# Kernel optimization log

Measured on AMD Instinct MI355X. Metric: run time of the kernel, lower is better.

Reference implementation:

```python
import jax, jax.numpy as jnp
import numpy as np
from jax import lax

# Paraformer-large streaming decoder dims
L, H, DFF, NH, DK, K, V, T, S, CKV, LB = 16, 512, 2048, 4, 128, 11, 8404, 64, 2048, 256, 256


def _ln(x, g, b, eps=1e-5):
    m = jnp.mean(x, axis=-1, keepdims=True)
    var = jnp.mean((x - m) ** 2, axis=-1, keepdims=True)
    return (x - m) * lax.rsqrt(var + eps) * g + b


def setup_inputs() -> dict:
    key = jax.random.key(0)
    ks = jax.random.split(key, 20)
    w = lambda k, shp: jax.random.normal(k, shp, jnp.float32) * 0.02
    return {
        "encoder_out": jax.random.normal(ks[0], (1, S, H), jnp.float32),
        "list_frame": jax.random.normal(ks[1], (1, T, H), jnp.float32),
        "fsmn_cache": jax.random.normal(ks[2], (L, 1, H, K - 1), jnp.float32),
        "key_cache": jax.random.normal(ks[3], (L, NH, DK, CKV), jnp.float32),
        "value_cache": jax.random.normal(ks[4], (L, NH, CKV, DK), jnp.float32),
        "norm1_g": jnp.ones((L, H)), "norm1_b": jnp.zeros((L, H)),
        "norm2_g": jnp.ones((L, H)), "norm2_b": jnp.zeros((L, H)),
        "norm3_g": jnp.ones((L, H)), "norm3_b": jnp.zeros((L, H)),
        "ffn_norm_g": jnp.ones((L, DFF)), "ffn_norm_b": jnp.zeros((L, DFF)),
        "w1": w(ks[5], (L, H, DFF)), "b1": jnp.zeros((L, DFF)),
        "w2": w(ks[6], (L, DFF, H)),  # bias-free in FunASR DecoderSANM
        "fsmn_w": w(ks[7], (L, H, K)),  # depthwise conv, groups=H, no bias
        "qw": w(ks[8], (L, H, H)), "qb": jnp.zeros((L, H)),
        "kvw": w(ks[9], (L, H, 2 * H)), "kvb": jnp.zeros((L, 2 * H)),
        "ow": w(ks[10], (L, H, H)), "ob": jnp.zeros((L, H)),
        "d3_norm1_g": jnp.ones((H,)), "d3_norm1_b": jnp.zeros((H,)),
        "d3_w1": w(ks[11], (H, DFF)), "d3_b1": jnp.zeros((DFF,)),
        "d3_ffn_norm_g": jnp.ones((DFF,)), "d3_ffn_norm_b": jnp.zeros((DFF,)),
        "d3_w2": w(ks[12], (DFF, H)),
        "after_norm_g": jnp.ones((H,)), "after_norm_b": jnp.zeros((H,)),
        "out_w": w(ks[13], (H, V)), "out_b": jnp.zeros((V,)),
        "list_frame_len": T,
    }


def reference(encoder_out, list_frame, fsmn_cache, key_cache, value_cache,
              norm1_g, norm1_b, norm2_g, norm2_b, norm3_g, norm3_b,
              ffn_norm_g, ffn_norm_b, w1, b1, w2, fsmn_w, qw, qb, kvw, kvb, ow, ob,
              d3_norm1_g, d3_norm1_b, d3_w1, d3_b1, d3_ffn_norm_g, d3_ffn_norm_b, d3_w2,
              after_norm_g, after_norm_b, out_w, out_b, list_frame_len):
    enc = encoder_out[0]  # [S, H]
    scale = DK ** -0.5

    def layer_fn(lf, p):
        (fc, kc, vc, n1g, n1b, n2g, n2b, n3g, n3b, fng, fnb,
         W1, B1, W2, FW, QW, QB, KVW, KVB, OW, OB) = p
        residual = lf
        y = _ln(lf, n1g, n1b)
        y = _ln(jax.nn.relu(y @ W1 + B1), fng, fnb) @ W2
        y = _ln(y, n2g, n2b)
        # cache concat; slice [look_back:] with look_back = -(K-1)-T keeps all K-1+T cols
        x_cat = jnp.concatenate([fc, jnp.swapaxes(y, 1, 2)], axis=-1)  # [1, H, K-1+T]
        conv = lax.conv_general_dilated(
            x_cat, FW[:, None, :], (1,), 'VALID',
            dimension_numbers=('NCH', 'OIH', 'NCH'), feature_group_count=H)  # [1, H, T]
        x = jnp.swapaxes(conv, 1, 2) + y + residual
        residual = x
        q = (_ln(x, n3g, n3b)[0] @ QW + QB).reshape(-1, NH, DK).transpose(1, 0, 2) * scale  # [h, T, dk]
        kv = enc @ KVW + KVB  # [S, 2H]
        k = kv[:, :H].reshape(-1, NH, DK).transpose(1, 2, 0)  # [h, dk, S]
        v = kv[:, H:].reshape(-1, NH, DK).transpose(1, 0, 2)  # [h, S, dk]
        k = jnp.concatenate([kc, k], axis=2)  # [h, dk, CKV+S]
        v = jnp.concatenate([vc, v], axis=1)  # [h, CKV+S, dk]
        attn = jax.nn.softmax(jnp.einsum('htd,hds->hts', q, k), axis=-1)
        ctx = jnp.einsum('hts,hsd->htd', attn, v).transpose(1, 0, 2).reshape(1, -1, H)
        lf = residual + ctx @ OW + OB
        return lf, (x_cat, k[:, :, -LB:], v[:, -LB:, :])

    layer_params = (fsmn_cache, key_cache, value_cache, norm1_g, norm1_b, norm2_g, norm2_b,
                    norm3_g, norm3_b, ffn_norm_g, ffn_norm_b, w1, b1, w2, fsmn_w,
                    qw, qb, kvw, kvb, ow, ob)
    lf, (save_fsmn, save_keys, save_values) = lax.scan(layer_fn, list_frame, layer_params)
    x = _ln(lf, d3_norm1_g, d3_norm1_b)
    x = _ln(jax.nn.relu(x @ d3_w1 + d3_b1), d3_ffn_norm_g, d3_ffn_norm_b) @ d3_w2
    logits = _ln(x, after_norm_g, after_norm_b) @ out_w + out_b
    max_logit_ids = jnp.argmax(logits, axis=-1).astype(jnp.int32)
    return save_fsmn, save_keys, save_values, max_logit_ids
```

## Files before the change

### kernel.cpp

```cpp
#include <hip/hip_runtime.h>

constexpr int LAY = 16, HID = 512, FF = 2048, NHD = 4, DKH = 128, KW = 11,
              VOC = 8404, TT = 64, SEQ = 2048, LBN = 256;

#define SWZ(row, e) ((e) ^ ((((row) >> 2) & 7) << 2))

__global__ void diag_k(float* __restrict__ p, float v) { p[threadIdx.x] = v; }

__global__ __launch_bounds__(256) void redln_k(
    const float* __restrict__ P, int N, int nch,
    const float* __restrict__ bias, const float* __restrict__ res, int relu,
    const float* __restrict__ g, const float* __restrict__ b,
    float* __restrict__ out1, float* __restrict__ out2) {
  __shared__ float buf[2048];
  __shared__ float red[256];
  const int m = blockIdx.x, tid = threadIdx.x;
  float s = 0.f;
  for (int n = tid; n < N; n += 256) {
    const float* p = P + (size_t)m * N + n;
    float v = 0.f;
    for (int c = 0; c < nch; ++c) v += p[(size_t)c * 64 * N];
    if (bias) v += bias[n];
    if (res) v += res[(size_t)m * N + n];
    if (relu) v = fmaxf(v, 0.f);
    if (out1) out1[(size_t)m * N + n] = v;
    buf[n] = v; s += v;
  }
  red[tid] = s; __syncthreads();
  for (int st = 128; st > 0; st >>= 1) { if (tid < st) red[tid] += red[tid + st]; __syncthreads(); }
  const float mean = red[0] / N;
  __syncthreads();
  float vs = 0.f;
  for (int n = tid; n < N; n += 256) { float d = buf[n] - mean; vs += d * d; }
  red[tid] = vs; __syncthreads();
  for (int st = 128; st > 0; st >>= 1) { if (tid < st) red[tid] += red[tid + st]; __syncthreads(); }
  const float inv = rsqrtf(red[0] / N + 1e-5f);
  for (int n = tid; n < N; n += 256)
    out2[(size_t)m * N + n] = (buf[n] - mean) * inv * g[n] + b[n];
}

__global__ __launch_bounds__(256) void gemm32_nn(
    const float* __restrict__ A, int lda, long sA,
    const float* __restrict__ B, int ldb, long sB,
    int N, int Kd, int nch,
    float* __restrict__ part, long pzs, int coff,
    int aCh, long aChS,
    const float* __restrict__ rsA, const float* __restrict__ bvA, long pzA) {
  __shared__ float As[64][64];
  __shared__ float Bs[64][40];
  const int tid = threadIdx.x;
  const int l16r = tid >> 4, l16c = tid & 15;
  const int lr = tid >> 3, lc = tid & 7;
  const int bn = blockIdx.x * 32;
  const int chunk = blockIdx.y;
  const int z = blockIdx.z;
  A += (long)z * sA; B += (long)z * sB;
  float acc[2][4] = {};
  const int ktiles = Kd >> 6;
  const int fa = (l16c & 7) << 2;
  for (int kt = chunk; kt < ktiles; kt += nch) {
    const int k0 = kt << 6;
    __syncthreads();
#pragma unroll
    for (int i = 0; i < 4; ++i) {
      const int r = l16r + 16 * i;
      float4 av;
      if (rsA) {
        const int kcol = k0 + l16c * 4;
        const int zz = kcol >> 7, d = kcol & 127;
        const float* ap = A + (size_t)zz * pzA + (size_t)r * 128 + d;
        av = *(const float4*)ap;
        for (int c = 1; c < aCh; ++c) {
          const float4 t2 = *(const float4*)(ap + (size_t)c * aChS);
          av.x += t2.x; av.y += t2.y; av.z += t2.z; av.w += t2.w;
        }
        const float4 bb = *(const float4*)(bvA + kcol);
        const float rv = rsA[zz * 64 + r];
        av.x += rv * bb.x; av.y += rv * bb.y; av.z += rv * bb.z; av.w += rv * bb.w;
      } else {
        const float* ap = A + (size_t)r * lda + k0 + l16c * 4;
        av = *(const float4*)ap;
        for (int c = 1; c < aCh; ++c) {
          const float4 t2 = *(const float4*)(ap + (size_t)c * aChS);
          av.x += t2.x; av.y += t2.y; av.z += t2.z; av.w += t2.w;
        }
      }
      As[l16c * 4 + 0][r ^ fa] = av.x; As[l16c * 4 + 1][r ^ fa] = av.y;
      As[l16c * 4 + 2][r ^ fa] = av.z; As[l16c * 4 + 3][r ^ fa] = av.w;
    }
#pragma unroll
    for (int i = 0; i < 2; ++i) {
      const int rb = lr + 32 * i;
      const float4 bv = *(const float4*)(B + (size_t)(k0 + rb) * ldb + bn + lc * 4);
      *(float4*)(&Bs[rb][lc * 4]) = bv;
    }
    __syncthreads();
#pragma unroll 8
    for (int kk = 0; kk < 64; ++kk) {
      const int fk = ((kk >> 2) & 7) << 2;
      const float2 a = *(const float2*)(&As[kk][(lr * 2) ^ fk]);
      const float4 b = *(const float4*)(&Bs[kk][lc * 4]);
      acc[0][0] += a.x * b.x; acc[0][1] += a.x * b.y; acc[0][2] += a.x * b.z; acc[0][3] += a.x * b.w;
      acc[1][0] += a.y * b.x; acc[1][1] += a.y * b.y; acc[1][2] += a.y * b.z; acc[1][3] += a.y * b.w;
    }
  }
  float* P = part + (size_t)z * pzs + (size_t)(coff + chunk) * 64 * N;
#pragma unroll
  for (int i = 0; i < 2; ++i) {
    const int m = lr * 2 + i;
#pragma unroll
    for (int j = 0; j < 4; ++j) P[(size_t)m * N + bn + lc * 4 + j] = acc[i][j];
  }
}

__global__ __launch_bounds__(256) void gemm_nn(
    const float* __restrict__ A, int lda, long sA,
    const float* __restrict__ B, int ldb, long sB,
    float* __restrict__ C, int ldc, long sC,
    const float* __restrict__ bias,
    const float* __restrict__ res, int ldres,
    int N, int Kd, int flags, int nch,
    float* __restrict__ part, long pzs, int coff,
    int aCh, long aChS) {
  __shared__ float As[64][64];
  __shared__ float Bs[64][64];
  const int tid = threadIdx.x;
  const int lr = tid >> 4, lc = tid & 15;
  const int bn = blockIdx.x * 64;
  const int chunk = blockIdx.y;
  const int z = blockIdx.z;
  A += (long)z * sA; B += (long)z * sB; C += (long)z * sC;
  float acc[4][4] = {};
  const int ktiles = Kd >> 6;
  const int fa = (lc & 7) << 2;
  for (int kt = chunk; kt < ktiles; kt += nch) {
    const int k0 = kt << 6;
    __syncthreads();
#pragma unroll
    for (int i = 0; i < 4; ++i) {
      const int r = lr + 16 * i;
      const float* ap = A + (size_t)r * lda + k0 + lc * 4;
      float4 av = *(const float4*)ap;
      for (int c = 1; c < aCh; ++c) {
        const float4 t2 = *(const float4*)(ap + (size_t)c * aChS);
        av.x += t2.x; av.y += t2.y; av.z += t2.z; av.w += t2.w;
      }
      As[lc * 4 + 0][r ^ fa] = av.x; As[lc * 4 + 1][r ^ fa] = av.y;
      As[lc * 4 + 2][r ^ fa] = av.z; As[lc * 4 + 3][r ^ fa] = av.w;
      const int n = bn + lc * 4;
      const float* bp = B + (size_t)(k0 + r) * ldb + n;
      float4 bv;
      if (n + 3 < N) bv = *(const float4*)bp;
      else {
        bv.x = (n + 0 < N) ? bp[0] : 0.f;
        bv.y = (n + 1 < N) ? bp[1] : 0.f;
        bv.z = (n + 2 < N) ? bp[2] : 0.f;
        bv.w = (n + 3 < N) ? bp[3] : 0.f;
      }
      *(float4*)(&Bs[r][SWZ(r, lc * 4)]) = bv;
    }
    __syncthreads();
#pragma unroll 8
    for (int kk = 0; kk < 64; ++kk) {
      const int fk = ((kk >> 2) & 7) << 2;
      const float4 a = *(const float4*)(&As[kk][(lr * 4) ^ fk]);
      const float4 b = *(const float4*)(&Bs[kk][(lc * 4) ^ fk]);
      acc[0][0] += a.x * b.x; acc[0][1] += a.x * b.y; acc[0][2] += a.x * b.z; acc[0][3] += a.x * b.w;
      acc[1][0] += a.y * b.x; acc[1][1] += a.y * b.y; acc[1][2] += a.y * b.z; acc[1][3] += a.y * b.w;
      acc[2][0] += a.z * b.x; acc[2][1] += a.z * b.y; acc[2][2] += a.z * b.z; acc[2][3] += a.z * b.w;
      acc[3][0] += a.w * b.x; acc[3][1] += a.w * b.y; acc[3][2] += a.w * b.z; acc[3][3] += a.w * b.w;
    }
  }
  if (part) {
    float* P = part + (size_t)z * pzs + (size_t)(coff + chunk) * 64 * N;
#pragma unroll
    for (int i = 0; i < 4; ++i) {
      const int m = lr * 4 + i;
#pragma unroll
      for (int j = 0; j < 4; ++j) P[(size_t)m * N + bn + lc * 4 + j] = acc[i][j];
    }
    return;
  }
#pragma unroll
  for (int i = 0; i < 4; ++i) {
    const int m = lr * 4 + i;
#pragma unroll
    for (int j = 0; j < 4; ++j) {
      const int n = bn + lc * 4 + j;
      if (n < N) {
        float v = acc[i][j];
        if (bias) v += bias[n];
        if (res) v += res[(size_t)m * ldres + n];
        if (flags & 2) v += C[(size_t)m * ldc + n];
        if (flags & 1) v = fmaxf(v, 0.f);
        C[(size_t)m * ldc + n] = v;
      }
    }
  }
}

__global__ __launch_bounds__(256) void gemm_nt(
    const float* __restrict__ A, int lda, long sA,
    const float* __restrict__ B, int ldb, long sB,
    float* __restrict__ C, int ldc, long sC,
    int N, int Kd, int nch, float* __restrict__ part) {
  __shared__ float As[64][64];
  __shared__ float Bs[64][64];
  const int tid = threadIdx.x;
  const int lr = tid >> 4, lc = tid & 15;
  const int bn = blockIdx.x * 64;
  const int chunk = blockIdx.y;
  const int z = blockIdx.z;
  A += (long)z * sA; B += (long)z * sB; C += (long)z * sC;
  float acc[4][4] = {};
  const int ktiles = Kd >> 6;
  const int fa = (lc & 7) << 2;
  for (int kt = chunk; kt < ktiles; kt += nch) {
    const int k0 = kt << 6;
    __syncthreads();
#pragma unroll
    for (int i = 0; i < 4; ++i) {
      const int r = lr + 16 * i;
      const float4 av = *(const float4*)(A + (size_t)r * lda + k0 + lc * 4);
      As[lc * 4 + 0][r ^ fa] = av.x; As[lc * 4 + 1][r ^ fa] = av.y;
      As[lc * 4 + 2][r ^ fa] = av.z; As[lc * 4 + 3][r ^ fa] = av.w;
      const float4 bv = *(const float4*)(B + (size_t)(bn + r) * ldb + k0 + lc * 4);
      Bs[lc * 4 + 0][r ^ fa] = bv.x; Bs[lc * 4 + 1][r ^ fa] = bv.y;
      Bs[lc * 4 + 2][r ^ fa] = bv.z; Bs[lc * 4 + 3][r ^ fa] = bv.w;
    }
    __syncthreads();
#pragma unroll 8
    for (int kk = 0; kk < 64; ++kk) {
      const int fk = ((kk >> 2) & 7) << 2;
      const float4 a = *(const float4*)(&As[kk][(lr * 4) ^ fk]);
      const float4 b = *(const float4*)(&Bs[kk][(lc * 4) ^ fk]);
      acc[0][0] += a.x * b.x; acc[0][1] += a.x * b.y; acc[0][2] += a.x * b.z; acc[0][3] += a.x * b.w;
      acc[1][0] += a.y * b.x; acc[1][1] += a.y * b.y; acc[1][2] += a.y * b.z; acc[1][3] += a.y * b.w;
      acc[2][0] += a.z * b.x; acc[2][1] += a.z * b.y; acc[2][2] += a.z * b.z; acc[2][3] += a.z * b.w;
      acc[3][0] += a.w * b.x; acc[3][1] += a.w * b.y; acc[3][2] += a.w * b.z; acc[3][3] += a.w * b.w;
    }
  }
  if (chunk == 0) {
#pragma unroll
    for (int i = 0; i < 4; ++i)
#pragma unroll
      for (int j = 0; j < 4; ++j)
        C[(size_t)(lr * 4 + i) * ldc + bn + lc * 4 + j] = acc[i][j];
  } else {
    float* P = part + (size_t)z * (64L * SEQ) + (size_t)(chunk - 1) * 64 * SEQ * NHD;
#pragma unroll
    for (int i = 0; i < 4; ++i)
#pragma unroll
      for (int j = 0; j < 4; ++j)
        P[(size_t)(lr * 4 + i) * SEQ + bn + lc * 4 + j] = acc[i][j];
  }
}

__global__ __launch_bounds__(256) void attn1_k(
    const float* __restrict__ qpart, const float* __restrict__ qbi_l,
    const float* __restrict__ Wkv, const float* __restrict__ kcl,
    float* __restrict__ qp, float* __restrict__ sc,
    int ckv, int sct) {
  __shared__ float As[64][64];
  __shared__ float Bs[64][64];
  const int tid = threadIdx.x;
  const int lr = tid >> 4, lc = tid & 15;
  const int h = blockIdx.z;
  const bool isQp = blockIdx.x < 8;
  const int bn = (isQp ? blockIdx.x : blockIdx.x - 8) * 64;
  const int fa = (lc & 7) << 2;
  float acc[4][4] = {};
  for (int k0 = 0; k0 < DKH; k0 += 64) {
    __syncthreads();
#pragma unroll
    for (int i = 0; i < 4; ++i) {
      const int r = lr + 16 * i;
      const float* ap = qpart + (size_t)r * HID + h * DKH + k0 + lc * 4;
      float4 av = *(const float4*)ap;
      for (int c = 1; c < 8; ++c) {
        const float4 t2 = *(const float4*)(ap + (size_t)c * 64 * HID);
        av.x += t2.x; av.y += t2.y; av.z += t2.z; av.w += t2.w;
      }
      const float4 bb = *(const float4*)(qbi_l + h * DKH + k0 + lc * 4);
      av.x += bb.x; av.y += bb.y; av.z += bb.z; av.w += bb.w;
      As[lc * 4 + 0][r ^ fa] = av.x; As[lc * 4 + 1][r ^ fa] = av.y;
      As[lc * 4 + 2][r ^ fa] = av.z; As[lc * 4 + 3][r ^ fa] = av.w;
      if (isQp) {
        const float4 bv = *(const float4*)(Wkv + (size_t)(bn + r) * (2 * HID) + h * DKH + k0 + lc * 4);
        Bs[lc * 4 + 0][r ^ fa] = bv.x; Bs[lc * 4 + 1][r ^ fa] = bv.y;
        Bs[lc * 4 + 2][r ^ fa] = bv.z; Bs[lc * 4 + 3][r ^ fa] = bv.w;
      } else {
        const float4 bv = *(const float4*)(kcl + ((size_t)h * DKH + k0 + r) * ckv + bn + lc * 4);
        *(float4*)(&Bs[r][SWZ(r, lc * 4)]) = bv;
      }
    }
    __syncthreads();
#pragma unroll 8
    for (int kk = 0; kk < 64; ++kk) {
      const int fk = ((kk >> 2) & 7) << 2;
      const float4 a = *(const float4*)(&As[kk][(lr * 4) ^ fk]);
      const float4 b = *(const float4*)(&Bs[kk][(lc * 4) ^ fk]);
      acc[0][0] += a.x * b.x; acc[0][1] += a.x * b.y; acc[0][2] += a.x * b.z; acc[0][3] += a.x * b.w;
      acc[1][0] += a.y * b.x; acc[1][1] += a.y * b.y; acc[1][2] += a.y * b.z; acc[1][3] += a.y * b.w;
      acc[2][0] += a.z * b.x; acc[2][1] += a.z * b.y; acc[2][2] += a.z * b.z; acc[2][3] += a.z * b.w;
      acc[3][0] += a.w * b.x; acc[3][1] += a.w * b.y; acc[3][2] += a.w * b.z; acc[3][3] += a.w * b.w;
    }
  }
  if (isQp) {
    float* C = qp + (size_t)h * TT * HID;
#pragma unroll
    for (int i = 0; i < 4; ++i)
#pragma unroll
      for (int j = 0; j < 4; ++j)
        C[(size_t)(lr * 4 + i) * HID + bn + lc * 4 + j] = acc[i][j];
  } else {
    float* C = sc + (size_t)h * TT * sct;
#pragma unroll
    for (int i = 0; i < 4; ++i)
#pragma unroll
      for (int j = 0; j < 4; ++j)
        C[(size_t)(lr * 4 + i) * sct + bn + lc * 4 + j] = acc[i][j];
  }
}

__global__ __launch_bounds__(256) void attn2_k(
    const float* __restrict__ sc, const float* __restrict__ vcl,
    const float* __restrict__ enc,
    float* __restrict__ part, float* __restrict__ partE,
    int ckv, int sct, int ncho, long pzc) {
  __shared__ float As[64][64];
  __shared__ float Bs[64][64];
  const int tid = threadIdx.x;
  const int lr = tid >> 4, lc = tid & 15;
  const int h = blockIdx.z;
  const int by = blockIdx.y;
  const bool isOld = blockIdx.x < 2;
  if (isOld && by >= ncho) return;
  if (!isOld && by >= 8) return;
  const float* A;
  const float* Bb;
  int lda, ldb, N, ktiles, nch, bn;
  float* P;
  if (isOld) {
    A = sc + (size_t)h * TT * sct;  lda = sct;
    Bb = vcl + (size_t)h * ckv * DKH; ldb = DKH;
    N = DKH; ktiles = ckv >> 6; nch = ncho; bn = blockIdx.x * 64;
    P = part + (size_t)h * pzc + (size_t)by * 64 * DKH;
  } else {
    A = sc + ckv + (size_t)h * TT * sct; lda = sct;
    Bb = enc; ldb = HID;
    N = HID; ktiles = SEQ >> 6; nch = 8; bn = (blockIdx.x - 2) * 64;
    P = partE + (size_t)h * (8L * 64 * HID) + (size_t)by * 64 * HID;
  }
  const int fa = (lc & 7) << 2;
  float acc[4][4] = {};
  for (int kt = by; kt < ktiles; kt += nch) {
    const int k0 = kt << 6;
    __syncthreads();
#pragma unroll
    for (int i = 0; i < 4; ++i) {
      const int r = lr + 16 * i;
      const float4 av = *(const float4*)(A + (size_t)r * lda + k0 + lc * 4);
      As[lc * 4 + 0][r ^ fa] = av.x; As[lc * 4 + 1][r ^ fa] = av.y;
      As[lc * 4 + 2][r ^ fa] = av.z; As[lc * 4 + 3][r ^ fa] = av.w;
      const float4 bv = *(const float4*)(Bb + (size_t)(k0 + r) * ldb + bn + lc * 4);
      *(float4*)(&Bs[r][SWZ(r, lc * 4)]) = bv;
    }
    __syncthreads();
#pragma unroll 8
    for (int kk = 0; kk < 64; ++kk) {
      const int fk = ((kk >> 2) & 7) << 2;
      const float4 a = *(const float4*)(&As[kk][(lr * 4) ^ fk]);
      const float4 b = *(const float4*)(&Bs[kk][(lc * 4) ^ fk]);
      acc[0][0] += a.x * b.x; acc[0][1] += a.x * b.y; acc[0][2] += a.x * b.z; acc[0][3] += a.x * b.w;
      acc[1][0] += a.y * b.x; acc[1][1] += a.y * b.y; acc[1][2] += a.y * b.z; acc[1][3] += a.y * b.w;
      acc[2][0] += a.z * b.x; acc[2][1] += a.z * b.y; acc[2][2] += a.z * b.z; acc[2][3] += a.z * b.w;
      acc[3][0] += a.w * b.x; acc[3][1] += a.w * b.y; acc[3][2] += a.w * b.z; acc[3][3] += a.w * b.w;
    }
  }
#pragma unroll
  for (int i = 0; i < 4; ++i)
#pragma unroll
    for (int j = 0; j < 4; ++j)
      P[(size_t)(lr * 4 + i) * N + bn + lc * 4 + j] = acc[i][j];
}

__global__ __launch_bounds__(256) void fsmnln_k(
    const float* __restrict__ y4, const float* __restrict__ lfin,
    const float* __restrict__ cache, const float* __restrict__ fw,
    const float* __restrict__ g, const float* __restrict__ b,
    float* __restrict__ xb, float* __restrict__ xcat,
    float* __restrict__ y1out) {
  __shared__ float buf[HID];
  __shared__ float red[256];
  const int t = blockIdx.x, tid = threadIdx.x;
  float s = 0.f;
  for (int h = tid; h < HID; h += 256) {
    float conv = 0.f;
#pragma unroll
    for (int k = 0; k < KW; ++k) {
      const int j = t + k;
      const float xcv = (j < KW - 1) ? cache[h * (KW - 1) + j]
                                     : y4[(size_t)(j - (KW - 1)) * HID + h];
      conv += xcv * fw[h * KW + k];
    }
    const float yv = y4[(size_t)t * HID + h];
    const float x = conv + yv + lfin[(size_t)t * HID + h];
    xb[(size_t)t * HID + h] = x;
    buf[h] = x; s += x;
    xcat[h * (KW - 1 + TT) + (KW - 1) + t] = yv;
    if (t == 0) {
      for (int j2 = 0; j2 < KW - 1; ++j2)
        xcat[h * (KW - 1 + TT) + j2] = cache[h * (KW - 1) + j2];
    }
  }
  red[tid] = s; __syncthreads();
  for (int st = 128; st > 0; st >>= 1) { if (tid < st) red[tid] += red[tid + st]; __syncthreads(); }
  const float mean = red[0] / HID;
  __syncthreads();
  float vs = 0.f;
  for (int h = tid; h < HID; h += 256) { float d = buf[h] - mean; vs += d * d; }
  red[tid] = vs; __syncthreads();
  for (int st = 128; st > 0; st >>= 1) { if (tid < st) red[tid] += red[tid + st]; __syncthreads(); }
  const float inv = rsqrtf(red[0] / HID + 1e-5f);
  for (int h = tid; h < HID; h += 256)
    y1out[(size_t)t * HID + h] = (buf[h] - mean) * inv * g[h] + b[h];
}

__global__ __launch_bounds__(256) void softmax_k(
    float* __restrict__ sc, float* __restrict__ rs,
    const float* __restrict__ qpart, const float* __restrict__ qbi_l,
    const float* __restrict__ kb, const float* __restrict__ partN,
    int cols, int newStart, float alpha) {
  __shared__ float srow[8192];
  __shared__ float red[256];
  const int tid = threadIdx.x;
  const int row = blockIdx.x;
  const int h = row >> 6, t = row & 63;
  sc += (size_t)row * cols;
  const float* pn = partN + (size_t)h * 64 * SEQ + (size_t)t * SEQ;
  float qv = 0.f;
  if (tid < DKH) {
    const float* qp0 = qpart + (size_t)t * HID + h * DKH + tid;
    float q = qp0[0];
    for (int c = 1; c < 8; ++c) q += qp0[(size_t)c * 64 * HID];
    q += qbi_l[h * DKH + tid];
    qv = q * kb[h * DKH + tid];
  }
  red[tid] = qv; __syncthreads();
  for (int st = 64; st > 0; st >>= 1) { if (tid < st) red[tid] += red[tid + st]; __syncthreads(); }
  const float qcv = red[0];
  __syncthreads();
  float m = -3.4e38f;
  for (int c = tid; c < cols; c += 256) {
    float v = sc[c];
    if (c >= newStart) v += pn[c - newStart] + qcv;
    v *= alpha;
    srow[c] = v; m = fmaxf(m, v);
  }
  red[tid] = m; __syncthreads();
  for (int st = 128; st > 0; st >>= 1) { if (tid < st) red[tid] = fmaxf(red[tid], red[tid + st]); __syncthreads(); }
  m = red[0]; __syncthreads();
  float s = 0.f;
  for (int c = tid; c < cols; c += 256) {
    const float e = __expf(srow[c] - m);
    srow[c] = e; s += e;
  }
  red[tid] = s; __syncthreads();
  for (int st = 128; st > 0; st >>= 1) { if (tid < st) red[tid] += red[tid + st]; __syncthreads(); }
  const float inv = 1.f / red[0];
  float ns = 0.f;
  for (int c = tid; c < cols; c += 256) {
    const float p = srow[c] * inv; sc[c] = p;
    if (c >= newStart) ns += p;
  }
  __syncthreads();
  red[tid] = ns; __syncthreads();
  for (int st = 128; st > 0; st >>= 1) { if (tid < st) red[tid] += red[tid + st]; __syncthreads(); }
  if (tid == 0) rs[row] = red[0];
}

__global__ __launch_bounds__(256) void argmax_k(const float* __restrict__ lg,
                                                float* __restrict__ out) {
  __shared__ float vs[256];
  __shared__ int ix[256];
  const int tid = threadIdx.x;
  lg += (size_t)blockIdx.x * VOC;
  float bm = -3.4e38f;
  int bi = 0;
  for (int c = tid; c < VOC; c += 256) { float v = lg[c]; if (v > bm) { bm = v; bi = c; } }
  vs[tid] = bm; ix[tid] = bi; __syncthreads();
  for (int st = 128; st > 0; st >>= 1) {
    if (tid < st) {
      if (vs[tid + st] > vs[tid] || (vs[tid + st] == vs[tid] && ix[tid + st] < ix[tid])) {
        vs[tid] = vs[tid + st]; ix[tid] = ix[tid + st];
      }
    }
    __syncthreads();
  }
  if (tid == 0) out[blockIdx.x] = (float)ix[0];
}

__global__ __launch_bounds__(256) void kvsave_k(const float* __restrict__ enc,
                                                const float* __restrict__ kvw,
                                                const float* __restrict__ kvb,
                                                float* __restrict__ keys,
                                                float* __restrict__ vals) {
  __shared__ float As[64][64];
  __shared__ float Bs[64][64];
  const int tid = threadIdx.x;
  const int lr = tid >> 4, lc = tid & 15;
  const int bn = blockIdx.x * 64, bm = blockIdx.y * 64;
  const int l = blockIdx.z;
  const float* W = kvw + (size_t)l * HID * 2 * HID;
  const int fa = (lc & 7) << 2;
  float acc[4][4] = {};
  for (int k0 = 0; k0 < HID; k0 += 64) {
    __syncthreads();
#pragma unroll
    for (int i = 0; i < 4; ++i) {
      const int r = lr + 16 * i;
      const float4 av =
          *(const float4*)(enc + (size_t)(SEQ - LBN + bm + r) * HID + k0 + lc * 4);
      As[lc * 4 + 0][r ^ fa] = av.x; As[lc * 4 + 1][r ^ fa] = av.y;
      As[lc * 4 + 2][r ^ fa] = av.z; As[lc * 4 + 3][r ^ fa] = av.w;
      const float4 bv = *(const float4*)(W + (size_t)(k0 + r) * (2 * HID) + bn + lc * 4);
      *(float4*)(&Bs[r][SWZ(r, lc * 4)]) = bv;
    }
    __syncthreads();
#pragma unroll 8
    for (int kk = 0; kk < 64; ++kk) {
      const int fk = ((kk >> 2) & 7) << 2;
      const float4 a = *(const float4*)(&As[kk][(lr * 4) ^ fk]);
      const float4 b = *(const float4*)(&Bs[kk][(lc * 4) ^ fk]);
      acc[0][0] += a.x * b.x; acc[0][1] += a.x * b.y; acc[0][2] += a.x * b.z; acc[0][3] += a.x * b.w;
      acc[1][0] += a.y * b.x; acc[1][1] += a.y * b.y; acc[1][2] += a.y * b.z; acc[1][3] += a.y * b.w;
      acc[2][0] += a.z * b.x; acc[2][1] += a.z * b.y; acc[2][2] += a.z * b.z; acc[2][3] += a.z * b.w;
      acc[3][0] += a.w * b.x; acc[3][1] += a.w * b.y; acc[3][2] += a.w * b.z; acc[3][3] += a.w * b.w;
    }
  }
#pragma unroll
  for (int i = 0; i < 4; ++i) {
    const int m = bm + lr * 4 + i;
#pragma unroll
    for (int j = 0; j < 4; ++j) {
      const int n = bn + lc * 4 + j;
      const float v = acc[i][j] + kvb[(size_t)l * 2 * HID + n];
      if (n < 512) {
        const int h = n >> 7, d = n & 127;
        keys[(((size_t)l * NHD + h) * DKH + d) * LBN + m] = v;
      } else {
        const int c = n - 512, h = c >> 7, d = c & 127;
        vals[(((size_t)l * NHD + h) * LBN + m) * DKH + d] = v;
      }
    }
  }
}

extern "C" void kernel_launch(void* const* d_in, const int* in_sizes, int n_in,
                              void* d_out, int out_size, void* d_ws, size_t ws_size,
                              hipStream_t stream) {
  static const int EXPECT[34] = {
      1048576, 32768, 81920, -1, -1,
      8192, 8192, 8192, 8192, 8192, 8192,
      32768, 32768,
      16777216, 32768, 16777216, 90112,
      4194304, 8192, 8388608, 16384, 4194304, 8192,
      512, 512, 1048576, 2048, 2048, 2048, 1048576,
      512, 512, 4302848, 8404};
  if (out_size != 4800576) {
    diag_k<<<1, 64, 0, stream>>>((float*)d_out, 9800000.f);
    return;
  }
  float* out_fsmn = (float*)d_out;
  float* out_keys = out_fsmn + (size_t)LAY * HID * (KW - 1 + TT);
  float* out_vals = out_keys + (size_t)LAY * NHD * DKH * LBN;
  float* out_ids  = out_vals + (size_t)LAY * NHD * LBN * DKH;
  if (n_in < 34) {
    diag_k<<<1, 64, 0, stream>>>(out_ids, 9900000.f);
    return;
  }
  for (int i = 0; i < 34; ++i) {
    if (EXPECT[i] >= 0 && in_sizes[i] != EXPECT[i]) {
      diag_k<<<1, 64, 0, stream>>>(out_ids, (float)((i + 1) * 100000));
      return;
    }
  }
  const long per = (long)LAY * NHD * DKH;
  const long ckl = (long)in_sizes[3] / per;
  if ((long)in_sizes[3] != ckl * per || in_sizes[4] != in_sizes[3] ||
      ckl <= 0 || (ckl & 63) != 0 || ckl > 6144) {
    diag_k<<<1, 64, 0, stream>>>(out_fsmn, (float)in_sizes[3]);
    return;
  }
  if (ws_size < (size_t)3145728 * 4) {
    diag_k<<<1, 64, 0, stream>>>(out_fsmn, 1.0e6f + (float)(ws_size >> 20));
    return;
  }
  const int ckv = (int)ckl;
  const int sct = ckv + SEQ;
  const long TS = (long)TT * sct;
  const int ncho = (ckv / 64 < 8) ? (ckv / 64) : 8;

  const float* enc    = (const float*)d_in[0];
  const float* lfrm   = (const float*)d_in[1];
  const float* fcache = (const float*)d_in[2];
  const float* kcache = (const float*)d_in[3];
  const float* vcache = (const float*)d_in[4];
  const float* n1g = (const float*)d_in[5];  const float* n1b = (const float*)d_in[6];
  const float* n2g = (const float*)d_in[7];  const float* n2b = (const float*)d_in[8];
  const float* n3g = (const float*)d_in[9];  const float* n3b = (const float*)d_in[10];
  const float* fng = (const float*)d_in[11]; const float* fnb = (const float*)d_in[12];
  const float* w1  = (const float*)d_in[13]; const float* b1  = (const float*)d_in[14];
  const float* w2  = (const float*)d_in[15];
  const float* fw  = (const float*)d_in[16];
  const float* qw  = (const float*)d_in[17]; const float* qbi  = (const float*)d_in[18];
  const float* kvw = (const float*)d_in[19]; const float* kvbi = (const float*)d_in[20];
  const float* ow  = (const float*)d_in[21]; const float* obi  = (const float*)d_in[22];
  const float* d3n1g = (const float*)d_in[23]; const float* d3n1b = (const float*)d_in[24];
  const float* d3w1  = (const float*)d_in[25]; const float* d3b1  = (const float*)d_in[26];
  const float* d3fng = (const float*)d_in[27]; const float* d3fnb = (const float*)d_in[28];
  const float* d3w2  = (const float*)d_in[29];
  const float* ang   = (const float*)d_in[30]; const float* anb = (const float*)d_in[31];
  const float* outw  = (const float*)d_in[32]; const float* outb = (const float*)d_in[33];

  float* sc  = out_keys;
  float* ov  = out_vals;
  float* lf  = ov + 0;
  float* y1  = ov + 32768;
  float* y4  = ov + 98304;
  float* xb  = ov + 131072;
  float* y2  = ov + 360448;
  float* qp  = ov + 491520;
  float* rs  = ov + 753920;
  float* lg  = ov + 754176;
  float* wsf   = (float*)d_ws;
  float* part  = wsf;
  float* part2 = wsf + 524288;
  float* partE = wsf + 1048576;
  float* partN = wsf + 2097152;

  const float alpha = 0.08838834764831845f;
  const long TH = (long)TT * HID;
  const long pz_ctx = (long)(ncho + 4) * 64 * DKH;

  redln_k<<<TT, 256, 0, stream>>>(lfrm, HID, 1, nullptr, nullptr, 0,
                                  n1g, n1b, lf, y1);

  for (int l = 0; l < LAY; ++l) {
    const float* Wkv = kvw + (size_t)l * HID * 2 * HID;
    const float* Bkv = kvbi + (size_t)l * 2 * HID;
    const float* qbi_l = qbi + (size_t)l * HID;
    gemm32_nn<<<dim3(64, 8, 1), 256, 0, stream>>>(
        y1, HID, 0, w1 + (size_t)l * HID * FF, FF, 0, FF, HID, 8, part2, 0, 0,
        1, 0, nullptr, nullptr, 0);
    redln_k<<<TT, 256, 0, stream>>>(part2, FF, 8, b1 + (size_t)l * FF, nullptr, 1,
                                    fng + (size_t)l * FF, fnb + (size_t)l * FF,
                                    nullptr, y2);
    gemm32_nn<<<dim3(16, 32, 1), 256, 0, stream>>>(
        y2, FF, 0, w2 + (size_t)l * FF * HID, HID, 0, HID, FF, 32, part2, 0, 0,
        1, 0, nullptr, nullptr, 0);
    redln_k<<<TT, 256, 0, stream>>>(part2, HID, 32, nullptr, nullptr, 0,
                                    n2g + l * HID, n2b + l * HID, nullptr, y4);
    fsmnln_k<<<TT, 256, 0, stream>>>(y4, lf, fcache + (size_t)l * HID * (KW - 1),
                                     fw + (size_t)l * HID * KW,
                                     n3g + l * HID, n3b + l * HID,
                                     xb, out_fsmn + (size_t)l * HID * (KW - 1 + TT), y1);
    gemm32_nn<<<dim3(16, 8, 1), 256, 0, stream>>>(
        y1, HID, 0, qw + (size_t)l * HID * HID, HID, 0, HID, HID, 8, part2, 0, 0,
        1, 0, nullptr, nullptr, 0);
    attn1_k<<<dim3(8 + ckv / 64, 1, NHD), 256, 0, stream>>>(
        part2, qbi_l, Wkv, kcache + (size_t)l * NHD * DKH * ckv, qp, sc, ckv, sct);
    gemm_nt<<<dim3(32, 2, NHD), 256, 0, stream>>>(
        qp, HID, TH, enc, HID, 0, sc + ckv, sct, TS, SEQ, HID, 2, partN);
    softmax_k<<<NHD * TT, 256, 0, stream>>>(sc, rs, part2, qbi_l, Bkv, partN,
                                            sct, ckv, alpha);
    attn2_k<<<dim3(10, 8, NHD), 256, 0, stream>>>(
        sc, vcache + (size_t)l * NHD * ckv * DKH, enc, part, partE,
        ckv, sct, ncho, pz_ctx);
    gemm32_nn<<<dim3(4, 4, NHD), 256, 0, stream>>>(
        partE, HID, 8L * 64 * HID, Wkv + HID, 2 * HID, DKH, DKH, HID, 4,
        part, pz_ctx, ncho, 8, 64L * HID, nullptr, nullptr, 0);
    gemm32_nn<<<dim3(16, 8, 1), 256, 0, stream>>>(
        part, 0, 0, ow + (size_t)l * HID * HID, HID, 0, HID, HID, 8, part2, 0, 0,
        ncho + 4, 8192, rs, Bkv + HID, pz_ctx);
    const float* ng = (l + 1 < LAY) ? n1g + (l + 1) * HID : d3n1g;
    const float* nb = (l + 1 < LAY) ? n1b + (l + 1) * HID : d3n1b;
    redln_k<<<TT, 256, 0, stream>>>(part2, HID, 8, obi + (size_t)l * HID, xb, 0,
                                    ng, nb, lf, y1);
  }

  gemm32_nn<<<dim3(64, 8, 1), 256, 0, stream>>>(
      y1, HID, 0, d3w1, FF, 0, FF, HID, 8, part2, 0, 0, 1, 0, nullptr, nullptr, 0);
  redln_k<<<TT, 256, 0, stream>>>(part2, FF, 8, d3b1, nullptr, 1,
                                  d3fng, d3fnb, nullptr, y2);
  gemm32_nn<<<dim3(16, 32, 1), 256, 0, stream>>>(
      y2, FF, 0, d3w2, HID, 0, HID, FF, 32, part2, 0, 0, 1, 0, nullptr, nullptr, 0);
  redln_k<<<TT, 256, 0, stream>>>(part2, HID, 32, nullptr, nullptr, 0,
                                  ang, anb, nullptr, y4);
  gemm_nn<<<dim3((VOC + 63) / 64, 1, 1), 256, 0, stream>>>(
      y4, HID, 0, outw, VOC, 0, lg, VOC, 0, outb, nullptr, 0,
      VOC, HID, 0, 1, nullptr, 0, 0, 1, 0);
  argmax_k<<<TT, 256, 0, stream>>>(lg, out_ids);

  kvsave_k<<<dim3(2 * HID / 64, LBN / 64, LAY), 256, 0, stream>>>(
      enc, kvw, kvbi, out_keys, out_vals);
}
```

Before: 2.928 ms.

## Overlap KV-cache save on a second stream and split-K the vocab projection

Moves the per-layer scratch buffers from the output key/value arrays into workspace, so the kvsave kernel can run on a forked non-blocking stream concurrently with the decoder layers. The final vocab GEMM is split into two K-chunks written as partials, and the argmax kernel fuses the partial sum and bias add. The costs are creating a stream and events on every call, a larger workspace requirement, and contention for compute units between the overlapped kernels.

```diff
diff --git a/kernel.cpp b/kernel.cpp
--- a/kernel.cpp
+++ b/kernel.cpp
@@ -177,7 +177,10 @@
     for (int i = 0; i < 4; ++i) {
       const int m = lr * 4 + i;
 #pragma unroll
-      for (int j = 0; j < 4; ++j) P[(size_t)m * N + bn + lc * 4 + j] = acc[i][j];
+      for (int j = 0; j < 4; ++j) {
+        const int n = bn + lc * 4 + j;
+        if (n < N) P[(size_t)m * N + n] = acc[i][j];
+      }
     }
     return;
   }
@@ -480,15 +483,21 @@
   if (tid == 0) rs[row] = red[0];
 }
 
-__global__ __launch_bounds__(256) void argmax_k(const float* __restrict__ lg,
+__global__ __launch_bounds__(256) void argmax_k(const float* __restrict__ P0,
+                                                const float* __restrict__ P1,
+                                                const float* __restrict__ bias,
                                                 float* __restrict__ out) {
   __shared__ float vs[256];
   __shared__ int ix[256];
   const int tid = threadIdx.x;
-  lg += (size_t)blockIdx.x * VOC;
+  P0 += (size_t)blockIdx.x * VOC;
+  P1 += (size_t)blockIdx.x * VOC;
   float bm = -3.4e38f;
   int bi = 0;
-  for (int c = tid; c < VOC; c += 256) { float v = lg[c]; if (v > bm) { bm = v; bi = c; } }
+  for (int c = tid; c < VOC; c += 256) {
+    const float v = P0[c] + P1[c] + bias[c];
+    if (v > bm) { bm = v; bi = c; }
+  }
   vs[tid] = bm; ix[tid] = bi; __syncthreads();
   for (int st = 128; st > 0; st >>= 1) {
     if (tid < st) {
@@ -593,7 +602,7 @@
     diag_k<<<1, 64, 0, stream>>>(out_fsmn, (float)in_sizes[3]);
     return;
   }
-  if (ws_size < (size_t)3145728 * 4) {
+  if (ws_size < (size_t)8388608 * 4) {
     diag_k<<<1, 64, 0, stream>>>(out_fsmn, 1.0e6f + (float)(ws_size >> 20));
     return;
   }
@@ -624,21 +633,21 @@
   const float* ang   = (const float*)d_in[30]; const float* anb = (const float*)d_in[31];
   const float* outw  = (const float*)d_in[32]; const float* outb = (const float*)d_in[33];
 
-  float* sc  = out_keys;
-  float* ov  = out_vals;
-  float* lf  = ov + 0;
-  float* y1  = ov + 32768;
-  float* y4  = ov + 98304;
-  float* xb  = ov + 131072;
-  float* y2  = ov + 360448;
-  float* qp  = ov + 491520;
-  float* rs  = ov + 753920;
-  float* lg  = ov + 754176;
   float* wsf   = (float*)d_ws;
   float* part  = wsf;
   float* part2 = wsf + 524288;
   float* partE = wsf + 1048576;
   float* partN = wsf + 2097152;
+  float* vp    = wsf + 2621440;
+  float* sb    = wsf + 3697152;
+  float* lf  = sb + 0;
+  float* y1  = sb + 32768;
+  float* y4  = sb + 65536;
+  float* xb  = sb + 98304;
+  float* y2  = sb + 131072;
+  float* qp  = sb + 163840;
+  float* rs  = sb + 294912;
+  float* sc  = sb + 295168;
 
   const float alpha = 0.08838834764831845f;
   const long TH = (long)TT * HID;
@@ -646,6 +655,17 @@
 
   redln_k<<<TT, 256, 0, stream>>>(lfrm, HID, 1, nullptr, nullptr, 0,
                                   n1g, n1b, lf, y1);
+
+  hipStream_t s2;
+  hipStreamCreateWithFlags(&s2, hipStreamNonBlocking);
+  hipEvent_t evFork, evKv;
+  hipEventCreateWithFlags(&evFork, hipEventDisableTiming);
+  hipEventCreateWithFlags(&evKv, hipEventDisableTiming);
+  hipEventRecord(evFork, stream);
+  hipStreamWaitEvent(s2, evFork, 0);
+  kvsave_k<<<dim3(2 * HID / 64, LBN / 64, LAY), 256, 0, s2>>>(
+      enc, kvw, kvbi, out_keys, out_vals);
+  hipEventRecord(evKv, s2);
 
   for (int l = 0; l < LAY; ++l) {
     const float* Wkv = kvw + (size_t)l * HID * 2 * HID;
@@ -698,11 +718,10 @@
       y2, FF, 0, d3w2, HID, 0, HID, FF, 32, part2, 0, 0, 1, 0, nullptr, nullptr, 0);
   redln_k<<<TT, 256, 0, stream>>>(part2, HID, 32, nullptr, nullptr, 0,
                                   ang, anb, nullptr, y4);
-  gemm_nn<<<dim3((VOC + 63) / 64, 1, 1), 256, 0, stream>>>(
-      y4, HID, 0, outw, VOC, 0, lg, VOC, 0, outb, nullptr, 0,
-      VOC, HID, 0, 1, nullptr, 0, 0, 1, 0);
-  argmax_k<<<TT, 256, 0, stream>>>(lg, out_ids);
-
-  kvsave_k<<<dim3(2 * HID / 64, LBN / 64, LAY), 256, 0, stream>>>(
-      enc, kvw, kvbi, out_keys, out_vals);
-}
+  gemm_nn<<<dim3((VOC + 63) / 64, 2, 1), 256, 0, stream>>>(
+      y4, HID, 0, outw, VOC, 0, nullptr, 0, 0, nullptr, nullptr, 0,
+      VOC, HID, 0, 2, vp, 0, 0, 1, 0);
+  argmax_k<<<TT, 256, 0, stream>>>(vp, vp + 64L * VOC, outb, out_ids);
+
+  hipStreamWaitEvent(stream, evKv, 0);
+}
```

After: 3.062 ms. 1.05x slower.
